# Performance work log

Hardware: AMD Instinct MI355X
Metric: run time of the kernel (lower is better)

## Reference

```python
import jax, jax.numpy as jnp
import numpy as np

B, S, E, H = 2, 2048, 1024, 16
DH = E // H            # 64 head dim
ROT = DH // 2          # 32: RotaryEmbedding(head_dim//2) rotates first 32 dims only
CTX = 2048             # sliding KV window
THETA = 10000.0


def setup_inputs() -> dict:
    key = jax.random.key(0)
    ks = jax.random.split(key, 7)
    sc = 1.0 / np.sqrt(E)
    mk = lambda k, sh, s=1.0: (jax.random.normal(k, sh, jnp.float32) * s)
    return {
        "query": mk(ks[0], (B, S, E)),
        "key":   mk(ks[1], (B, S, E)),
        "value": mk(ks[2], (B, S, E)),
        "Wq": mk(ks[3], (E, E), sc), "bq": jnp.zeros((E,), jnp.float32),
        "Wk": mk(ks[4], (E, E), sc), "bk": jnp.zeros((E,), jnp.float32),
        "Wv": mk(ks[5], (E, E), sc), "bv": jnp.zeros((E,), jnp.float32),
        "Wo": mk(ks[6], (E, E), sc), "bo": jnp.zeros((E,), jnp.float32),
    }


def _rope(t):
    # t: [B, H, S, DH]; rotate first ROT dims, pass the rest through (offset=0).
    seq = t.shape[2]
    inv_freq = 1.0 / (THETA ** (jnp.arange(0, ROT, 2, dtype=jnp.float32) / ROT))  # [ROT//2]
    ang = jnp.arange(seq, dtype=jnp.float32)[:, None] * inv_freq[None, :]          # [S, ROT//2]
    cos = jnp.repeat(jnp.cos(ang), 2, axis=-1)  # [S, ROT] (pairwise-interleaved freqs)
    sin = jnp.repeat(jnp.sin(ang), 2, axis=-1)
    rot, rest = t[..., :ROT], t[..., ROT:]
    x1, x2 = rot[..., 0::2], rot[..., 1::2]
    rot_half = jnp.stack([-x2, x1], axis=-1).reshape(rot.shape)  # rotate_half on pairs
    return jnp.concatenate([rot * cos + rot_half * sin, rest], axis=-1)


def reference(query, key, value, Wq, bq, Wk, bk, Wv, bv, Wo, bo):
    def heads(x, W, b):
        return (x @ W.T + b).reshape(B, -1, H, DH).transpose(0, 2, 1, 3)  # [B,H,S,DH]

    q = _rope(heads(query, Wq, bq))
    k = _rope(heads(key, Wk, bk))
    v = heads(value, Wv, bv)
    k, v = k[:, :, -CTX:], v[:, :, -CTX:]  # sliding window (no-op when S == CTX)

    scale = jnp.float32(1.0 / np.sqrt(DH))
    scores = jnp.einsum('bhqd,bhkd->bhqk', q, k) * scale  # [B,H,Sq,Sk]
    sq, sk = q.shape[2], k.shape[2]
    causal = jnp.tril(jnp.ones((sk, sk), dtype=bool))[-sq:]  # [Sq,Sk]
    scores = jnp.where(causal[None, None], scores, jnp.float32(-jnp.inf))
    probs = jax.nn.softmax(scores, axis=-1)  # dropout=0 (eval)
    out = jnp.einsum('bhqk,bhkd->bhqd', probs, v)
    out = out.transpose(0, 2, 1, 3).reshape(B, -1, E)
    return out @ Wo.T + bo
```

## Files before the change

### kernel.cpp

```cpp
#include <hip/hip_runtime.h>
#include <stdint.h>
#include <math.h>

typedef __bf16 bf16x8 __attribute__((ext_vector_type(8)));
typedef float f32x4 __attribute__((ext_vector_type(4)));

__device__ __forceinline__ float bf2f(uint16_t x) {
  unsigned u = ((unsigned)x) << 16;
  float f;
  __builtin_memcpy(&f, &u, 4);
  return f;
}
__device__ __forceinline__ uint16_t f2bf(float f) {
  __bf16 h = (__bf16)f;
  uint16_t u;
  __builtin_memcpy(&u, &h, 2);
  return u;
}
__device__ __forceinline__ bf16x8 pack8(float4 lo, float4 hi) {
  bf16x8 v;
  v[0] = (__bf16)lo.x; v[1] = (__bf16)lo.y; v[2] = (__bf16)lo.z; v[3] = (__bf16)lo.w;
  v[4] = (__bf16)hi.x; v[5] = (__bf16)hi.y; v[6] = (__bf16)hi.z; v[7] = (__bf16)hi.w;
  return v;
}
__device__ __forceinline__ bf16x8 cvt8(const float* p) {
  return pack8(*(const float4*)p, *(const float4*)(p + 4));
}

typedef __attribute__((address_space(1))) const unsigned int gu32;
typedef __attribute__((address_space(3))) unsigned int lu32;
__device__ __forceinline__ void async_copy16(const void* gp, void* lp) {
  __builtin_amdgcn_global_load_lds((gu32*)gp, (lu32*)lp, 16, 0, 0);
}

__global__ __launch_bounds__(256) void cvt_kernel(
    const float* __restrict__ s0, uint16_t* __restrict__ d0,
    const float* __restrict__ s1, uint16_t* __restrict__ d1,
    const float* __restrict__ s2, uint16_t* __restrict__ d2,
    const float* __restrict__ s3, uint16_t* __restrict__ d3) {
  const int z = blockIdx.z;
  const float* s = z == 0 ? s0 : z == 1 ? s1 : z == 2 ? s2 : s3;
  uint16_t* d = z == 0 ? d0 : z == 1 ? d1 : z == 2 ? d2 : d3;
  const size_t idx = ((size_t)blockIdx.x * 256 + threadIdx.x) * 8;
  *(bf16x8*)(d + idx) = cvt8(s + idx);
}

template <bool A_F32, bool W_F32, bool C_F32, bool VT, bool ROPE, int BM, int NF>
__global__ __launch_bounds__(256) void gemm3_kernel(
    const void* __restrict__ A0, const void* __restrict__ W0,
    const float* __restrict__ b0, void* __restrict__ C0,
    const void* __restrict__ A1, const void* __restrict__ W1,
    const float* __restrict__ b1, void* __restrict__ C1,
    const void* __restrict__ A2, const void* __restrict__ W2,
    const float* __restrict__ b2, void* __restrict__ C2,
    int M, int N, int K) {
  constexpr int BN = NF * 32;
  constexpr int AF = BM / 32;
  const int z = blockIdx.z;
  const void* Av = z == 0 ? A0 : z == 1 ? A1 : A2;
  const void* Wp = z == 0 ? W0 : z == 1 ? W1 : W2;
  const float* bias = z == 0 ? b0 : z == 1 ? b1 : b2;
  void* Cv = z == 0 ? C0 : z == 1 ? C1 : C2;

  __shared__ __align__(16) uint16_t As[BM * 64];
  __shared__ __align__(16) uint16_t Bs[BN * 64];
  const int tid = threadIdx.x;
  const int wave = tid >> 6, lane = tid & 63;
  const int quad = lane >> 4, l16 = lane & 15;
  const int l = blockIdx.y * gridDim.x + blockIdx.x;
  const int nmt = M / BM;
  const int bm = (l % nmt) * BM;
  const int bn = (l / nmt) * BN;
  const int wm = (wave >> 1) * (BM / 2);
  const int wn = (wave & 1) * (BN / 2);

  f32x4 acc[AF][NF] = {};

  for (int k0 = 0; k0 < K; k0 += 64) {
    bf16x8 ar[AF], wr[NF];
    if (A_F32) {
#pragma unroll
      for (int i = 0; i < AF; i++) {
        const int c = i * 256 + tid;
        const int r = c >> 3, pc = ((c & 7) ^ (r & 7)) << 3;
        ar[i] = cvt8((const float*)Av + (size_t)(bm + r) * K + k0 + pc);
      }
    }
    if (W_F32) {
#pragma unroll
      for (int i = 0; i < NF; i++) {
        const int c = i * 256 + tid;
        const int r = c >> 3, pc = ((c & 7) ^ (r & 7)) << 3;
        wr[i] = cvt8((const float*)Wp + (size_t)(bn + r) * K + k0 + pc);
      }
    }
    if (k0) __syncthreads();
#pragma unroll
    for (int i = 0; i < AF; i++) {
      const int c = i * 256 + tid;
      const int r = c >> 3, pc = ((c & 7) ^ (r & 7)) << 3;
      if (A_F32) *(bf16x8*)(As + c * 8) = ar[i];
      else async_copy16((const uint16_t*)Av + (size_t)(bm + r) * K + k0 + pc,
                        As + (i * 256 + (tid & 192)) * 8);
    }
#pragma unroll
    for (int i = 0; i < NF; i++) {
      const int c = i * 256 + tid;
      const int r = c >> 3, pc = ((c & 7) ^ (r & 7)) << 3;
      if (W_F32) *(bf16x8*)(Bs + c * 8) = wr[i];
      else async_copy16((const uint16_t*)Wp + (size_t)(bn + r) * K + k0 + pc,
                        Bs + (i * 256 + (tid & 192)) * 8);
    }
    __syncthreads();
#pragma unroll
    for (int s = 0; s < 2; s++) {
      bf16x8 af[AF], bfr[NF];
#pragma unroll
      for (int i = 0; i < AF; i++) {
        const int Ra = wm + i * 16 + l16;
        af[i] = *(const bf16x8*)(As + Ra * 64 + (((s * 4 + quad) ^ (Ra & 7)) << 3));
      }
#pragma unroll
      for (int j = 0; j < NF; j++) {
        const int Rb = wn + j * 16 + l16;
        bfr[j] = *(const bf16x8*)(Bs + Rb * 64 + (((s * 4 + quad) ^ (Rb & 7)) << 3));
      }
#pragma unroll
      for (int i = 0; i < AF; i++)
#pragma unroll
        for (int j = 0; j < NF; j++)
          acc[i][j] = __builtin_amdgcn_mfma_f32_16x16x32_bf16(af[i], bfr[j], acc[i][j], 0, 0, 0);
    }
  }
  if (VT && z == 2) {
#pragma unroll
    for (int j = 0; j < NF; j++) {
      const int n = bn + wn + j * 16 + l16;
      const float bj = bias[n];
      const int h = n >> 6, dh = n & 63;
#pragma unroll
      for (int i = 0; i < AF; i++) {
        const int m0 = bm + wm + i * 16 + quad * 4;
        const int b = m0 >> 11, s0 = m0 & 2047;
        uint2 pk;
        pk.x = (unsigned)f2bf(acc[i][j][0] + bj) |
               ((unsigned)f2bf(acc[i][j][1] + bj) << 16);
        pk.y = (unsigned)f2bf(acc[i][j][2] + bj) |
               ((unsigned)f2bf(acc[i][j][3] + bj) << 16);
        *(uint2*)((uint16_t*)Cv + ((size_t)((b * 16 + h) * 64 + dh)) * 2048 + s0) = pk;
      }
    }
  } else {
#pragma unroll
    for (int j = 0; j < NF; j++) {
      const int n = bn + wn + j * 16 + l16;
      const float bj = bias[n];
      const int dh = (wn + j * 16 + l16) & 63;
      const bool rot = ROPE && (((wn + j * 16) & 63) < 32);
      float invrev = 0.f;
      if (rot)
        invrev = __expf(-0.5756462732485115f * (float)(dh >> 1)) *
                 0.15915494309189535f;
#pragma unroll
      for (int i = 0; i < AF; i++) {
        const int m0 = bm + wm + i * 16 + quad * 4;
#pragma unroll
        for (int r = 0; r < 4; r++) {
          float v = acc[i][j][r] + bj;
          if (rot) {
            const int s_pos = (m0 + r) & 2047;
            float rev = (float)s_pos * invrev;
            rev -= floorf(rev);
            const float sn = __builtin_amdgcn_sinf(rev);
            const float cs = __builtin_amdgcn_cosf(rev);
            const float partner = __shfl_xor(v, 1);
            v = (dh & 1) ? (v * cs + partner * sn) : (v * cs - partner * sn);
          }
          if (C_F32) ((float*)Cv)[(size_t)(m0 + r) * N + n] = v;
          else       ((uint16_t*)Cv)[(size_t)(m0 + r) * N + n] = f2bf(v);
        }
      }
    }
  }
}

template <bool SPLIT>
__global__ __launch_bounds__(256) void flash_kernel(const uint16_t* __restrict__ Q,
                                                    const uint16_t* __restrict__ K,
                                                    const uint16_t* __restrict__ VT,
                                                    uint16_t* __restrict__ AO,
                                                    float* __restrict__ Po,
                                                    float* __restrict__ Pl) {
  const int bx = blockIdx.x;
  const int xcd = bx & 7;
  int bh, qt2, half;
  if (SPLIT) {
    const int s7 = bx >> 3;
    const int grp = s7 >> 5;
    const int w = s7 & 31;
    bh = grp * 8 + xcd;
    const int qb = w & 15;
    qt2 = (grp & 1) ? qb : 15 - qb;
    half = w >> 4;
  } else {
    const int slot = bx >> 3;
    bh = (slot >> 4) * 8 + xcd;
    qt2 = (slot < 32) ? (15 - (slot & 15)) : (slot & 15);
    half = 0;
  }
  const int h = bh & 15;
  const int b = bh >> 4;
  const int tid = threadIdx.x;
  const int wave = tid >> 6, lane = tid & 63;
  const int quad = lane >> 4, l16 = lane & 15;

  __shared__ __align__(16) uint16_t Ks[64 * 64];
  __shared__ __align__(16) uint16_t Vt[64 * 64];
  __shared__ __align__(16) uint16_t Ps[4][32 * 72];

  const float QS = 0.18033688011112042f;
  const int qrow0 = qt2 * 128 + wave * 16 + l16;
  const int qrow1 = qrow0 + 64;
  bf16x8 qf0[2], qf1[2];
#pragma unroll
  for (int s = 0; s < 2; s++) {
    union { bf16x8 v; uint16_t u[8]; } t0, t1;
    t0.v = *(const bf16x8*)(Q + ((size_t)(b * 2048 + qrow0) * 1024) + h * 64 + s * 32 + quad * 8);
    t1.v = *(const bf16x8*)(Q + ((size_t)(b * 2048 + qrow1) * 1024) + h * 64 + s * 32 + quad * 8);
#pragma unroll
    for (int j = 0; j < 8; j++) {
      t0.u[j] = f2bf(bf2f(t0.u[j]) * QS);
      t1.u[j] = f2bf(bf2f(t1.u[j]) * QS);
    }
    qf0[s] = t0.v;
    qf1[s] = t1.v;
  }

  const size_t vbase = ((size_t)((b * 16 + h) * 64)) * 2048;

  float lsum0 = 0.f, lsum1 = 0.f;
  f32x4 o0[4] = {}, o1[4] = {};

  const int nkt = 2 * qt2 + 2;
  const int k0b = SPLIT ? half * (qt2 + 1) : 0;
  const int k0e = SPLIT ? (half + 1) * (qt2 + 1) : nkt;
  for (int kt = k0b; kt < k0e; kt++) {
    if (kt != k0b) __syncthreads();
#pragma unroll
    for (int i = 0; i < 2; i++) {
      const int c = i * 256 + tid;
      const int r = c >> 3, pc = ((c & 7) ^ (r & 7)) << 3;
      async_copy16(K + ((size_t)(b * 2048 + kt * 64 + r) * 1024) + h * 64 + pc,
                   Ks + (i * 256 + (tid & 192)) * 8);
      async_copy16(VT + vbase + (size_t)r * 2048 + kt * 64 + pc,
                   Vt + (i * 256 + (tid & 192)) * 8);
    }
    __syncthreads();

    const bool f0 = (kt < nkt - 1);

    {
      f32x4 sacc[4] = {};
#pragma unroll
      for (int s = 0; s < 2; s++)
#pragma unroll
        for (int t = 0; t < 4; t++) {
          const int R = t * 16 + l16;
          bf16x8 kf = *(const bf16x8*)(Ks + R * 64 + (((s * 4 + quad) ^ (R & 7)) << 3));
          sacc[t] = __builtin_amdgcn_mfma_f32_16x16x32_bf16(kf, qf1[s], sacc[t], 0, 0, 0);
        }
      if (kt == nkt - 1) {
#pragma unroll
        for (int t = 0; t < 4; t++)
#pragma unroll
          for (int r = 0; r < 4; r++)
            if (kt * 64 + t * 16 + quad * 4 + r > qrow1) sacc[t][r] = -1e30f;
      }
#pragma unroll
      for (int t = 0; t < 4; t++) {
        float p0 = __builtin_amdgcn_exp2f(sacc[t][0]);
        float p1 = __builtin_amdgcn_exp2f(sacc[t][1]);
        float p2 = __builtin_amdgcn_exp2f(sacc[t][2]);
        float p3 = __builtin_amdgcn_exp2f(sacc[t][3]);
        lsum1 += (p0 + p1) + (p2 + p3);
        uint2 pk;
        pk.x = (unsigned)f2bf(p0) | ((unsigned)f2bf(p1) << 16);
        pk.y = (unsigned)f2bf(p2) | ((unsigned)f2bf(p3) << 16);
        *(uint2*)(&Ps[wave][(16 + l16) * 72 + t * 16 + quad * 4]) = pk;
      }
    }
    if (f0) {
      f32x4 sacc[4] = {};
#pragma unroll
      for (int s = 0; s < 2; s++)
#pragma unroll
        for (int t = 0; t < 4; t++) {
          const int R = t * 16 + l16;
          bf16x8 kf = *(const bf16x8*)(Ks + R * 64 + (((s * 4 + quad) ^ (R & 7)) << 3));
          sacc[t] = __builtin_amdgcn_mfma_f32_16x16x32_bf16(kf, qf0[s], sacc[t], 0, 0, 0);
        }
      if (kt == nkt - 2) {
#pragma unroll
        for (int t = 0; t < 4; t++)
#pragma unroll
          for (int r = 0; r < 4; r++)
            if (kt * 64 + t * 16 + quad * 4 + r > qrow0) sacc[t][r] = -1e30f;
      }
#pragma unroll
      for (int t = 0; t < 4; t++) {
        float p0 = __builtin_amdgcn_exp2f(sacc[t][0]);
        float p1 = __builtin_amdgcn_exp2f(sacc[t][1]);
        float p2 = __builtin_amdgcn_exp2f(sacc[t][2]);
        float p3 = __builtin_amdgcn_exp2f(sacc[t][3]);
        lsum0 += (p0 + p1) + (p2 + p3);
        uint2 pk;
        pk.x = (unsigned)f2bf(p0) | ((unsigned)f2bf(p1) << 16);
        pk.y = (unsigned)f2bf(p2) | ((unsigned)f2bf(p3) << 16);
        *(uint2*)(&Ps[wave][l16 * 72 + t * 16 + quad * 4]) = pk;
      }
    }
#pragma unroll
    for (int s = 0; s < 2; s++) {
      const bf16x8 pa1 = *(const bf16x8*)(&Ps[wave][(16 + l16) * 72 + s * 32 + quad * 8]);
#pragma unroll
      for (int t = 0; t < 4; t++) {
        const int R = t * 16 + l16;
        const bf16x8 vb = *(const bf16x8*)(Vt + R * 64 + (((s * 4 + quad) ^ (R & 7)) << 3));
        o1[t] = __builtin_amdgcn_mfma_f32_16x16x32_bf16(pa1, vb, o1[t], 0, 0, 0);
      }
    }
    if (f0) {
#pragma unroll
      for (int s = 0; s < 2; s++) {
        const bf16x8 pa0 = *(const bf16x8*)(&Ps[wave][l16 * 72 + s * 32 + quad * 8]);
#pragma unroll
        for (int t = 0; t < 4; t++) {
          const int R = t * 16 + l16;
          const bf16x8 vb = *(const bf16x8*)(Vt + R * 64 + (((s * 4 + quad) ^ (R & 7)) << 3));
          o0[t] = __builtin_amdgcn_mfma_f32_16x16x32_bf16(pa0, vb, o0[t], 0, 0, 0);
        }
      }
    }
  }
  lsum0 += __shfl_xor(lsum0, 16);
  lsum0 += __shfl_xor(lsum0, 32);
  lsum1 += __shfl_xor(lsum1, 16);
  lsum1 += __shfl_xor(lsum1, 32);

  if (SPLIT) {
    const int pidx = (bh * 16 + qt2) * 2 + half;
    float* po = Po + (size_t)pidx * 8192;
#pragma unroll
    for (int t = 0; t < 4; t++)
#pragma unroll
      for (int r = 0; r < 4; r++) {
        const int row = wave * 16 + quad * 4 + r;
        po[row * 64 + t * 16 + l16] = o0[t][r];
        po[(row + 64) * 64 + t * 16 + l16] = o1[t][r];
      }
    if (lane < 16) {
      Pl[pidx * 128 + wave * 16 + l16] = lsum0;
      Pl[pidx * 128 + 64 + wave * 16 + l16] = lsum1;
    }
  } else {
    const float inv0 = 1.f / lsum0, inv1 = 1.f / lsum1;
    float invr0[4], invr1[4];
#pragma unroll
    for (int r = 0; r < 4; r++) {
      invr0[r] = __shfl(inv0, quad * 4 + r);
      invr1[r] = __shfl(inv1, quad * 4 + r);
    }
#pragma unroll
    for (int t = 0; t < 4; t++)
#pragma unroll
      for (int r = 0; r < 4; r++) {
        const int qg0 = qt2 * 128 + wave * 16 + quad * 4 + r;
        AO[((size_t)(b * 2048 + qg0) * 1024) + h * 64 + t * 16 + l16] =
            f2bf(o0[t][r] * invr0[r]);
        AO[((size_t)(b * 2048 + qg0 + 64) * 1024) + h * 64 + t * 16 + l16] =
            f2bf(o1[t][r] * invr1[r]);
      }
  }
}

__global__ __launch_bounds__(256) void combine_kernel(
    const float* __restrict__ Po, const float* __restrict__ Pl,
    uint16_t* __restrict__ AO) {
  const int cb = blockIdx.x;
  const int bh = cb >> 4, qt2 = cb & 15;
  const int b = bh >> 4, h = bh & 15;
  const int tid = threadIdx.x;
  const int row = tid >> 1;
  const int c0 = (tid & 1) * 32;
  const int p0 = (bh * 16 + qt2) * 2;
  const float inv = 1.f / (Pl[p0 * 128 + row] + Pl[(p0 + 1) * 128 + row]);
  const float* pa = Po + (size_t)p0 * 8192 + row * 64 + c0;
  const float* pb = pa + 8192;
  uint16_t* dst = AO + ((size_t)(b * 2048 + qt2 * 128 + row) * 1024) + h * 64 + c0;
#pragma unroll
  for (int i = 0; i < 4; i++) {
    const float4 a0 = ((const float4*)pa)[2 * i], a1 = ((const float4*)pa)[2 * i + 1];
    const float4 b0 = ((const float4*)pb)[2 * i], b1 = ((const float4*)pb)[2 * i + 1];
    bf16x8 v;
    v[0] = (__bf16)((a0.x + b0.x) * inv);
    v[1] = (__bf16)((a0.y + b0.y) * inv);
    v[2] = (__bf16)((a0.z + b0.z) * inv);
    v[3] = (__bf16)((a0.w + b0.w) * inv);
    v[4] = (__bf16)((a1.x + b1.x) * inv);
    v[5] = (__bf16)((a1.y + b1.y) * inv);
    v[6] = (__bf16)((a1.z + b1.z) * inv);
    v[7] = (__bf16)((a1.w + b1.w) * inv);
    *(bf16x8*)(dst + i * 8) = v;
  }
}

extern "C" void kernel_launch(void* const* d_in, const int* in_sizes, int n_in,
                              void* d_out, int out_size, void* d_ws, size_t ws_size,
                              hipStream_t stream) {
  const float* query = (const float*)d_in[0];
  const float* key   = (const float*)d_in[1];
  const float* value = (const float*)d_in[2];
  const float* Wq = (const float*)d_in[3];
  const float* bq = (const float*)d_in[4];
  const float* Wk = (const float*)d_in[5];
  const float* bk = (const float*)d_in[6];
  const float* Wv = (const float*)d_in[7];
  const float* bv = (const float*)d_in[8];
  const float* Wo = (const float*)d_in[9];
  const float* bo = (const float*)d_in[10];
  float* out = (float*)d_out;

  uint16_t* ws = (uint16_t*)d_ws;
  uint16_t* Qb  = ws;
  uint16_t* Kb  = ws + (size_t)4194304;
  uint16_t* VTb = ws + (size_t)8388608;

  dim3 blk(256);

  if (ws_size >= (size_t)64 * 1024 * 1024) {
    float*    Pl  = (float*)(ws + (size_t)12582912);
    uint16_t* Woc = ws + (size_t)12845056;
    uint16_t* Qc  = ws + (size_t)16777216;
    uint16_t* Kc  = ws + (size_t)20971520;
    uint16_t* Vc  = ws + (size_t)25165824;
    uint16_t* Wqc = ws + (size_t)29360128;
    uint16_t* Wkc = ws + (size_t)30408704;
    uint16_t* Wvc = ws + (size_t)31457280;
    float*    Po  = (float*)(ws + (size_t)16777216);
    uint16_t* AOc = ws;

    cvt_kernel<<<dim3(512, 1, 4), blk, 0, stream>>>(
        Wq, Wqc, Wk, Wkc, Wv, Wvc, Wo, Woc);
    cvt_kernel<<<dim3(2048, 1, 3), blk, 0, stream>>>(
        query, Qc, key, Kc, value, Vc, nullptr, nullptr);
    gemm3_kernel<false, false, false, true, true, 128, 4><<<dim3(8, 32, 3), blk, 0, stream>>>(
        Qc, Wqc, bq, Qb,
        Kc, Wkc, bk, Kb,
        Vc, Wvc, bv, VTb,
        4096, 1024, 1024);
    flash_kernel<true><<<dim3(1024), blk, 0, stream>>>(Qb, Kb, VTb, nullptr, Po, Pl);
    combine_kernel<<<dim3(512), blk, 0, stream>>>(Po, Pl, AOc);
    gemm3_kernel<false, false, true, false, false, 128, 2><<<dim3(16, 32, 1), blk, 0, stream>>>(
        AOc, Woc, bo, out,
        AOc, Woc, bo, out,
        AOc, Woc, bo, out,
        4096, 1024, 1024);
  } else {
    uint16_t* AOb = ws + (size_t)12582912;
    uint16_t* Wqc = AOb;
    uint16_t* Wkc = AOb + (size_t)1048576;
    uint16_t* Wvc = AOb + (size_t)2097152;
    cvt_kernel<<<dim3(512, 1, 3), blk, 0, stream>>>(
        Wq, Wqc, Wk, Wkc, Wv, Wvc, nullptr, nullptr);
    gemm3_kernel<true, false, false, true, true, 128, 2><<<dim3(16, 32, 3), blk, 0, stream>>>(
        query, Wqc, bq, Qb,
        key,   Wkc, bk, Kb,
        value, Wvc, bv, VTb,
        4096, 1024, 1024);
    flash_kernel<false><<<dim3(512), blk, 0, stream>>>(Qb, Kb, VTb, AOb, nullptr, nullptr);
    gemm3_kernel<false, true, true, false, false, 128, 2><<<dim3(16, 32, 1), blk, 0, stream>>>(
        AOb, Wo, bo, out,
        AOb, Wo, bo, out,
        AOb, Wo, bo, out,
        4096, 1024, 1024);
  }
}
```

Baseline: 228.0 us.

## Split flash attention KV range four ways and halve P scratch in LDS

```diff
diff --git a/kernel.cpp b/kernel.cpp
--- a/kernel.cpp
+++ b/kernel.cpp
@@ -184,29 +184,29 @@
   }
 }
 
-template <bool SPLIT>
-__global__ __launch_bounds__(256) void flash_kernel(const uint16_t* __restrict__ Q,
-                                                    const uint16_t* __restrict__ K,
-                                                    const uint16_t* __restrict__ VT,
-                                                    uint16_t* __restrict__ AO,
-                                                    float* __restrict__ Po,
-                                                    float* __restrict__ Pl) {
+template <int NS>
+__global__ __launch_bounds__(256, 6) void flash_kernel(
+    const uint16_t* __restrict__ Q, const uint16_t* __restrict__ K,
+    const uint16_t* __restrict__ VT, uint16_t* __restrict__ AO,
+    float* __restrict__ Po, float* __restrict__ Pl) {
   const int bx = blockIdx.x;
   const int xcd = bx & 7;
-  int bh, qt2, half;
-  if (SPLIT) {
-    const int s7 = bx >> 3;
-    const int grp = s7 >> 5;
-    const int w = s7 & 31;
+  const int s7 = bx >> 3;
+  int bh, qt2, seg;
+  if (NS == 1) {
+    bh = (s7 >> 4) * 8 + xcd;
+    qt2 = (s7 < 32) ? (15 - (s7 & 15)) : (s7 & 15);
+    seg = 0;
+  } else if (NS == 2) {
+    const int grp = s7 >> 5, w = s7 & 31;
     bh = grp * 8 + xcd;
-    const int qb = w & 15;
-    qt2 = (grp & 1) ? qb : 15 - qb;
-    half = w >> 4;
+    qt2 = (grp & 1) ? (w & 15) : (15 - (w & 15));
+    seg = w >> 4;
   } else {
-    const int slot = bx >> 3;
-    bh = (slot >> 4) * 8 + xcd;
-    qt2 = (slot < 32) ? (15 - (slot & 15)) : (slot & 15);
-    half = 0;
+    const int grp = s7 >> 5, w = s7 & 31;
+    bh = (grp & 3) * 8 + xcd;
+    qt2 = (grp & 1) ? (w & 15) : (15 - (w & 15));
+    seg = (w >> 4) * 2 + (grp >> 2);
   }
   const int h = bh & 15;
   const int b = bh >> 4;
@@ -216,7 +216,7 @@
 
   __shared__ __align__(16) uint16_t Ks[64 * 64];
   __shared__ __align__(16) uint16_t Vt[64 * 64];
-  __shared__ __align__(16) uint16_t Ps[4][32 * 72];
+  __shared__ __align__(16) uint16_t Ps[4][16 * 72];
 
   const float QS = 0.18033688011112042f;
   const int qrow0 = qt2 * 128 + wave * 16 + l16;
@@ -242,8 +242,8 @@
   f32x4 o0[4] = {}, o1[4] = {};
 
   const int nkt = 2 * qt2 + 2;
-  const int k0b = SPLIT ? half * (qt2 + 1) : 0;
-  const int k0e = SPLIT ? (half + 1) * (qt2 + 1) : nkt;
+  const int k0b = (NS == 1) ? 0 : seg * nkt / NS;
+  const int k0e = (NS == 1) ? nkt : (seg + 1) * nkt / NS;
   for (int kt = k0b; kt < k0e; kt++) {
     if (kt != k0b) __syncthreads();
 #pragma unroll
@@ -286,7 +286,17 @@
         uint2 pk;
         pk.x = (unsigned)f2bf(p0) | ((unsigned)f2bf(p1) << 16);
         pk.y = (unsigned)f2bf(p2) | ((unsigned)f2bf(p3) << 16);
-        *(uint2*)(&Ps[wave][(16 + l16) * 72 + t * 16 + quad * 4]) = pk;
+        *(uint2*)(&Ps[wave][l16 * 72 + t * 16 + quad * 4]) = pk;
+      }
+#pragma unroll
+      for (int s = 0; s < 2; s++) {
+        const bf16x8 pa = *(const bf16x8*)(&Ps[wave][l16 * 72 + s * 32 + quad * 8]);
+#pragma unroll
+        for (int t = 0; t < 4; t++) {
+          const int R = t * 16 + l16;
+          const bf16x8 vb = *(const bf16x8*)(Vt + R * 64 + (((s * 4 + quad) ^ (R & 7)) << 3));
+          o1[t] = __builtin_amdgcn_mfma_f32_16x16x32_bf16(pa, vb, o1[t], 0, 0, 0);
+        }
       }
     }
     if (f0) {
@@ -318,26 +328,14 @@
         pk.y = (unsigned)f2bf(p2) | ((unsigned)f2bf(p3) << 16);
         *(uint2*)(&Ps[wave][l16 * 72 + t * 16 + quad * 4]) = pk;
       }
-    }
-#pragma unroll
-    for (int s = 0; s < 2; s++) {
-      const bf16x8 pa1 = *(const bf16x8*)(&Ps[wave][(16 + l16) * 72 + s * 32 + quad * 8]);
-#pragma unroll
-      for (int t = 0; t < 4; t++) {
-        const int R = t * 16 + l16;
-        const bf16x8 vb = *(const bf16x8*)(Vt + R * 64 + (((s * 4 + quad) ^ (R & 7)) << 3));
-        o1[t] = __builtin_amdgcn_mfma_f32_16x16x32_bf16(pa1, vb, o1[t], 0, 0, 0);
-      }
-    }
-    if (f0) {
 #pragma unroll
       for (int s = 0; s < 2; s++) {
-        const bf16x8 pa0 = *(const bf16x8*)(&Ps[wave][l16 * 72 + s * 32 + quad * 8]);
+        const bf16x8 pa = *(const bf16x8*)(&Ps[wave][l16 * 72 + s * 32 + quad * 8]);
 #pragma unroll
         for (int t = 0; t < 4; t++) {
           const int R = t * 16 + l16;
           const bf16x8 vb = *(const bf16x8*)(Vt + R * 64 + (((s * 4 + quad) ^ (R & 7)) << 3));
-          o0[t] = __builtin_amdgcn_mfma_f32_16x16x32_bf16(pa0, vb, o0[t], 0, 0, 0);
+          o0[t] = __builtin_amdgcn_mfma_f32_16x16x32_bf16(pa, vb, o0[t], 0, 0, 0);
         }
       }
     }
@@ -347,8 +345,8 @@
   lsum1 += __shfl_xor(lsum1, 16);
   lsum1 += __shfl_xor(lsum1, 32);
 
-  if (SPLIT) {
-    const int pidx = (bh * 16 + qt2) * 2 + half;
+  if (NS > 1) {
+    const int pidx = (bh * 16 + qt2) * NS + seg;
     float* po = Po + (size_t)pidx * 8192;
 #pragma unroll
     for (int t = 0; t < 4; t++)
@@ -383,6 +381,7 @@
   }
 }
 
+template <int NS>
 __global__ __launch_bounds__(256) void combine_kernel(
     const float* __restrict__ Po, const float* __restrict__ Pl,
     uint16_t* __restrict__ AO) {
@@ -392,24 +391,27 @@
   const int tid = threadIdx.x;
   const int row = tid >> 1;
   const int c0 = (tid & 1) * 32;
-  const int p0 = (bh * 16 + qt2) * 2;
-  const float inv = 1.f / (Pl[p0 * 128 + row] + Pl[(p0 + 1) * 128 + row]);
-  const float* pa = Po + (size_t)p0 * 8192 + row * 64 + c0;
-  const float* pb = pa + 8192;
+  const int p0 = (bh * 16 + qt2) * NS;
+  float ls = 0.f;
+#pragma unroll
+  for (int j = 0; j < NS; j++) ls += Pl[(p0 + j) * 128 + row];
+  const float inv = 1.f / ls;
   uint16_t* dst = AO + ((size_t)(b * 2048 + qt2 * 128 + row) * 1024) + h * 64 + c0;
 #pragma unroll
   for (int i = 0; i < 4; i++) {
-    const float4 a0 = ((const float4*)pa)[2 * i], a1 = ((const float4*)pa)[2 * i + 1];
-    const float4 b0 = ((const float4*)pb)[2 * i], b1 = ((const float4*)pb)[2 * i + 1];
+    float a0 = 0, a1 = 0, a2 = 0, a3 = 0, a4 = 0, a5 = 0, a6 = 0, a7 = 0;
+#pragma unroll
+    for (int j = 0; j < NS; j++) {
+      const float* p = Po + (size_t)(p0 + j) * 8192 + row * 64 + c0 + i * 8;
+      const float4 x = ((const float4*)p)[0], y = ((const float4*)p)[1];
+      a0 += x.x; a1 += x.y; a2 += x.z; a3 += x.w;
+      a4 += y.x; a5 += y.y; a6 += y.z; a7 += y.w;
+    }
     bf16x8 v;
-    v[0] = (__bf16)((a0.x + b0.x) * inv);
-    v[1] = (__bf16)((a0.y + b0.y) * inv);
-    v[2] = (__bf16)((a0.z + b0.z) * inv);
-    v[3] = (__bf16)((a0.w + b0.w) * inv);
-    v[4] = (__bf16)((a1.x + b1.x) * inv);
-    v[5] = (__bf16)((a1.y + b1.y) * inv);
-    v[6] = (__bf16)((a1.z + b1.z) * inv);
-    v[7] = (__bf16)((a1.w + b1.w) * inv);
+    v[0] = (__bf16)(a0 * inv); v[1] = (__bf16)(a1 * inv);
+    v[2] = (__bf16)(a2 * inv); v[3] = (__bf16)(a3 * inv);
+    v[4] = (__bf16)(a4 * inv); v[5] = (__bf16)(a5 * inv);
+    v[6] = (__bf16)(a6 * inv); v[7] = (__bf16)(a7 * inv);
     *(bf16x8*)(dst + i * 8) = v;
   }
 }
@@ -438,8 +440,9 @@
   dim3 blk(256);
 
   if (ws_size >= (size_t)64 * 1024 * 1024) {
+    const bool big = ws_size >= (size_t)96 * 1024 * 1024;
     float*    Pl  = (float*)(ws + (size_t)12582912);
-    uint16_t* Woc = ws + (size_t)12845056;
+    uint16_t* Woc = ws + (size_t)13107200;
     uint16_t* Qc  = ws + (size_t)16777216;
     uint16_t* Kc  = ws + (size_t)20971520;
     uint16_t* Vc  = ws + (size_t)25165824;
@@ -458,8 +461,13 @@
         Kc, Wkc, bk, Kb,
         Vc, Wvc, bv, VTb,
         4096, 1024, 1024);
-    flash_kernel<true><<<dim3(1024), blk, 0, stream>>>(Qb, Kb, VTb, nullptr, Po, Pl);
-    combine_kernel<<<dim3(512), blk, 0, stream>>>(Po, Pl, AOc);
+    if (big) {
+      flash_kernel<4><<<dim3(2048), blk, 0, stream>>>(Qb, Kb, VTb, nullptr, Po, Pl);
+      combine_kernel<4><<<dim3(512), blk, 0, stream>>>(Po, Pl, AOc);
+    } else {
+      flash_kernel<2><<<dim3(1024), blk, 0, stream>>>(Qb, Kb, VTb, nullptr, Po, Pl);
+      combine_kernel<2><<<dim3(512), blk, 0, stream>>>(Po, Pl, AOc);
+    }
     gemm3_kernel<false, false, true, false, false, 128, 2><<<dim3(16, 32, 1), blk, 0, stream>>>(
         AOc, Woc, bo, out,
         AOc, Woc, bo, out,
@@ -477,7 +485,7 @@
         key,   Wkc, bk, Kb,
         value, Wvc, bv, VTb,
         4096, 1024, 1024);
-    flash_kernel<false><<<dim3(512), blk, 0, stream>>>(Qb, Kb, VTb, AOb, nullptr, nullptr);
+    flash_kernel<1><<<dim3(512), blk, 0, stream>>>(Qb, Kb, VTb, AOb, nullptr, nullptr);
     gemm3_kernel<false, true, true, false, false, 128, 2><<<dim3(16, 32, 1), blk, 0, stream>>>(
         AOb, Wo, bo, out,
         AOb, Wo, bo, out,
```

Result: slower. 323.4 us (+41.9%).
